# Kernel tuning notes

Measured on AMD Instinct MI355X. Metric: run time of the kernel, lower is better.

The kernel has to match this reference:

```python
import jax, jax.numpy as jnp
import numpy as np
from jax import lax

D, H_HEADS, DEPTH, E, HID, P, NCLS = 768, 12, 12, 4, 3072, 16, 1000

def _ln(x, w, b, eps=1e-5):
    m = x.mean(-1, keepdims=True)
    v = ((x - m) ** 2).mean(-1, keepdims=True)
    return (x - m) * lax.rsqrt(v + eps) * w + b

def setup_inputs() -> dict:
    key = jax.random.key(0)
    ks = jax.random.split(key, 16)
    s = 0.02
    inp = {
        'x': jax.random.normal(ks[0], (32, 3, 224, 224), jnp.float32),
        'conv_w': jax.random.normal(ks[1], (D, 3, P, P), jnp.float32) * s,
        'conv_b': jnp.zeros((D,), jnp.float32),
        'cls_token': jnp.zeros((1, 1, D), jnp.float32),
        'pos_embed': jax.random.normal(ks[2], (1, 197, D), jnp.float32) * s,
        'ln1_w': jnp.ones((DEPTH, D), jnp.float32),
        'ln1_b': jnp.zeros((DEPTH, D), jnp.float32),
        'qkv_w': jax.random.normal(ks[3], (DEPTH, 3 * D, D), jnp.float32) * s,
        'qkv_b': jnp.zeros((DEPTH, 3 * D), jnp.float32),
        'out_w': jax.random.normal(ks[4], (DEPTH, D, D), jnp.float32) * s,
        'out_b': jnp.zeros((DEPTH, D), jnp.float32),
        'ln2_w': jnp.ones((DEPTH, D), jnp.float32),
        'ln2_b': jnp.zeros((DEPTH, D), jnp.float32),
        'gate_w': jax.random.normal(ks[5], (DEPTH, E, D), jnp.float32) * s,
        'gate_b': jnp.zeros((DEPTH, E), jnp.float32),
        'e1_w': jax.random.normal(ks[6], (DEPTH, E, HID, D), jnp.float32) * s,
        'e1_b': jnp.zeros((DEPTH, E, HID), jnp.float32),
        'e2_w': jax.random.normal(ks[7], (DEPTH, E, D, HID), jnp.float32) * s,
        'e2_b': jnp.zeros((DEPTH, E, D), jnp.float32),
        'fnorm_w': jnp.ones((D,), jnp.float32),
        'fnorm_b': jnp.zeros((D,), jnp.float32),
        'head_w': jax.random.normal(ks[8], (NCLS, D), jnp.float32) * s,
        'head_b': jnp.zeros((NCLS,), jnp.float32),
    }
    return inp

def reference(x, conv_w, conv_b, cls_token, pos_embed, ln1_w, ln1_b, qkv_w, qkv_b,
              out_w, out_b, ln2_w, ln2_b, gate_w, gate_b, e1_w, e1_b, e2_w, e2_b,
              fnorm_w, fnorm_b, head_w, head_b):
    B = x.shape[0]
    # patch embedding: conv stride=patch, then flatten -> [B, N, D]
    x = lax.conv_general_dilated(x, conv_w, (P, P), 'VALID',
                                 dimension_numbers=('NCHW', 'OIHW', 'NCHW'))
    x = x + conv_b[None, :, None, None]
    x = x.reshape(B, D, -1).transpose(0, 2, 1)
    x = jnp.concatenate([jnp.broadcast_to(cls_token, (B, 1, D)), x], axis=1)
    x = x + pos_embed
    N = x.shape[1]
    hd = D // H_HEADS
    for i in range(DEPTH):
        # --- attention ---
        h = x
        y = _ln(x, ln1_w[i], ln1_b[i])
        qkv = y @ qkv_w[i].T + qkv_b[i]                      # [B,N,3D]
        q, k, v = jnp.split(qkv, 3, axis=-1)
        q = q.reshape(B, N, H_HEADS, hd).transpose(0, 2, 1, 3) / jnp.sqrt(hd).astype(x.dtype)
        k = k.reshape(B, N, H_HEADS, hd).transpose(0, 2, 1, 3)
        v = v.reshape(B, N, H_HEADS, hd).transpose(0, 2, 1, 3)
        attn = jax.nn.softmax(jnp.einsum('bhqd,bhkd->bhqk', q, k), axis=-1)
        ctx = jnp.einsum('bhqk,bhkd->bhqd', attn, v).transpose(0, 2, 1, 3).reshape(B, N, D)
        x = h + (ctx @ out_w[i].T + out_b[i])
        # --- MoE MLP (dense: all experts computed then masked, top_k=1) ---
        h = x
        y = _ln(x, ln2_w[i], ln2_b[i])
        gate = y @ gate_w[i].T + gate_b[i]                   # [B,N,E]
        topk_scores, topk_idx = lax.top_k(gate, 1)           # [B,N,1]
        score = jax.nn.softmax(topk_scores, axis=-1)[..., 0]  # [B,N] (==1 for k=1)
        h1 = jax.nn.gelu(jnp.einsum('bnd,ehd->benh', y, e1_w[i])
                         + e1_b[i][None, :, None, :], approximate=False)  # [B,E,N,HID]
        oe = jnp.einsum('benh,edh->bend', h1, e2_w[i]) + e2_b[i][None, :, None, :]
        mask = jax.nn.one_hot(topk_idx[..., 0], E, dtype=y.dtype)  # [B,N,E]
        moe = jnp.einsum('bne,bend->bnd', mask * score[..., None], oe)
        x = h + moe
    x = _ln(x, fnorm_w, fnorm_b)
    cls = x[:, 0]
    return cls @ head_w.T + head_b
```

## Files before the change

kernel.cpp:

```cpp
#include <hip/hip_runtime.h>
#include <hip/hip_bf16.h>
#include <math.h>

#define D_MODEL 768
#define SEQ     197
#define BATCH   32
#define NTOK    (BATCH*SEQ)
#define NHEAD   12
#define HDIM    64
#define NEXP    4
#define HID_N   3072
#define DEPTH_N 12

typedef __attribute__((ext_vector_type(4))) float f32x4;
typedef __attribute__((ext_vector_type(8))) short bf16x8;
typedef __attribute__((ext_vector_type(4))) unsigned short u16x4;
typedef unsigned short u16;

static __device__ __forceinline__ u16 f2bf(float f){
  unsigned int u = __builtin_bit_cast(unsigned int, f);
  u += 0x7FFFu + ((u >> 16) & 1u);
  return (u16)(u >> 16);
}
static __device__ __forceinline__ void split_bf(float x, u16& h, u16& l){
  h = f2bf(x);
  float hf = __builtin_bit_cast(float, (unsigned)h << 16);
  l = f2bf(x - hf);
}

static __device__ __forceinline__ float wred_sum(float v){
  #pragma unroll
  for (int off = 32; off; off >>= 1) v += __shfl_down(v, off);
  return v;
}

static __device__ __forceinline__ int xcd_map(int orig, int nwg){
  int q = nwg >> 3, r = nwg & 7;
  int xcd = orig & 7, idx = orig >> 3;
  return (xcd < r ? xcd*(q+1) : r*(q+1) + (xcd-r)*q) + idx;
}

static __device__ __forceinline__ void gld16(const u16* g, u16* l){
  __builtin_amdgcn_global_load_lds(
      (const __attribute__((address_space(1))) unsigned int*)g,
      (__attribute__((address_space(3))) unsigned int*)l, 16, 0, 0);
}

__global__ __launch_bounds__(256) void split_many(const float* __restrict__ src,
                                                  u16* __restrict__ hi,
                                                  u16* __restrict__ lo, long n4){
  for (long i = blockIdx.x*256L + threadIdx.x; i < n4; i += (long)gridDim.x*256){
    f32x4 v = *reinterpret_cast<const f32x4*>(src + i*4);
    u16x4 h, l;
    #pragma unroll
    for (int j = 0; j < 4; j++){ u16 hh, ll; split_bf(v[j], hh, ll); h[j]=hh; l[j]=ll; }
    *reinterpret_cast<u16x4*>(hi + i*4) = h;
    *reinterpret_cast<u16x4*>(lo + i*4) = l;
  }
}

template<int MODE>
__global__ __launch_bounds__(256, 2) void gemm_split(
    const u16* __restrict__ Ahp, const u16* __restrict__ Alp,
    const u16* __restrict__ Whp, const u16* __restrict__ Wlp,
    const float* __restrict__ bias, const float* __restrict__ resid,
    float* __restrict__ C, const float* __restrict__ pos,
    u16* __restrict__ Chi, u16* __restrict__ Clo,
    const int* __restrict__ toks, const int* __restrict__ cnts,
    const int* __restrict__ offs, const int* __restrict__ tiles,
    int M, int N, int K)
{
  const int tid = threadIdx.x;
  const int NB = N >> 7;
  const int nm = gridDim.x / NB;
  const int lg = xcd_map(blockIdx.x, gridDim.x);
  const int mt = lg % nm, nb = lg / nm;

  int cnt = M, base = 0, m0;
  if (MODE == 2 || MODE == 3){
    if (mt >= tiles[0]) return;
    const int e = tiles[1 + 2*mt];
    m0 = tiles[2 + 2*mt];
    cnt  = cnts[e];
    base = offs[e];
    Whp  += (size_t)e * N * K;
    Wlp  += (size_t)e * N * K;
    bias += (size_t)e * N;
  } else {
    m0 = mt * 128;
  }
  const int n0 = nb * 128;

  __shared__ __align__(16) u16 lds[2][4][4096];

  const int lane = tid & 63, wid = tid >> 6;
  const int i0 = wid*128 + lane;
  const int r0 = i0 >> 2, r1 = r0 + 16;
  const int x0 = (i0 & 3) ^ ((r0 >> 1) & 3);
  const int x1 = (i0 & 3) ^ ((r1 >> 1) & 3);
  const int d0 = wid*1024, d1 = wid*1024 + 512;

  size_t aA0 = 0, aA1 = 0, pb0 = 0, pb1 = 0;
  {
    const int gm0 = m0 + r0, gm1 = m0 + r1;
    if (MODE == 0 || MODE == 1){
      aA0 = (size_t)(gm0 < M ? gm0 : 0) * K + x0*8;
      aA1 = (size_t)(gm1 < M ? gm1 : 0) * K + x1*8;
    }
    if (MODE == 2){
      aA0 = (size_t)(gm0 < cnt ? toks[base+gm0] : 0) * K + x0*8;
      aA1 = (size_t)(gm1 < cnt ? toks[base+gm1] : 0) * K + x1*8;
    }
    if (MODE == 3){
      aA0 = (size_t)(gm0 < cnt ? base+gm0 : 0) * K + x0*8;
      aA1 = (size_t)(gm1 < cnt ? base+gm1 : 0) * K + x1*8;
    }
    if (MODE == 4){
      int b_ = gm0 / 196, pp = gm0 - b_*196;
      pb0 = (size_t)b_*150528 + (size_t)(pp/14)*3584 + (size_t)(pp%14)*16;
      b_ = gm1 / 196; pp = gm1 - b_*196;
      pb1 = (size_t)b_*150528 + (size_t)(pp/14)*3584 + (size_t)(pp%14)*16;
    }
  }
  const size_t aW0 = (size_t)(n0 + r0) * K + x0*8;
  const size_t aW1 = (size_t)(n0 + r1) * K + x1*8;

  auto STAGE = [&](int buf, int t){
    const int k0 = t * 32;
    if (MODE == 4){
      const int kq0 = k0 + x0*8, kq1 = k0 + x1*8;
      size_t a0 = pb0 + (size_t)(kq0>>8)*50176 + (size_t)((kq0>>4)&15)*224 + (size_t)(kq0&15);
      size_t a1 = pb1 + (size_t)(kq1>>8)*50176 + (size_t)((kq1>>4)&15)*224 + (size_t)(kq1&15);
      gld16(Ahp + a0, &lds[buf][0][d0]); gld16(Ahp + a1, &lds[buf][0][d1]);
      gld16(Alp + a0, &lds[buf][1][d0]); gld16(Alp + a1, &lds[buf][1][d1]);
    } else {
      gld16(Ahp + aA0 + k0, &lds[buf][0][d0]); gld16(Ahp + aA1 + k0, &lds[buf][0][d1]);
      gld16(Alp + aA0 + k0, &lds[buf][1][d0]); gld16(Alp + aA1 + k0, &lds[buf][1][d1]);
    }
    gld16(Whp + aW0 + k0, &lds[buf][2][d0]); gld16(Whp + aW1 + k0, &lds[buf][2][d1]);
    gld16(Wlp + aW0 + k0, &lds[buf][3][d0]); gld16(Wlp + aW1 + k0, &lds[buf][3][d1]);
  };

  const int wr = wid >> 1, wc = wid & 1;
  const int lr = lane & 15, lq = lane >> 4;
  int cA[4], cW[4];
  #pragma unroll
  for (int mi = 0; mi < 4; mi++){
    int ra = wr*64 + mi*16 + lr;
    cA[mi] = (4*ra + (lq ^ ((ra>>1)&3))) * 8;
  }
  #pragma unroll
  for (int nj = 0; nj < 4; nj++){
    int rw = wc*64 + nj*16 + lr;
    cW[nj] = (4*rw + (lq ^ ((rw>>1)&3))) * 8;
  }

  const int NT = K >> 5;
  f32x4 acc[4][4] = {};

  STAGE(0, 0);
  for (int t = 0; t < NT; t++){
    const int buf = t & 1;
    if (t + 1 < NT){
      STAGE(buf ^ 1, t + 1);
      asm volatile("s_waitcnt vmcnt(8)" ::: "memory");
    } else {
      asm volatile("s_waitcnt vmcnt(0)" ::: "memory");
    }
    __builtin_amdgcn_s_barrier();
    asm volatile("" ::: "memory");
    const u16* L = &lds[buf][0][0];
    bf16x8 afh[4], afl[4], bfh[4], bfl[4];
    #pragma unroll
    for (int mi = 0; mi < 4; mi++){
      afh[mi] = *reinterpret_cast<const bf16x8*>(L + cA[mi]);
      afl[mi] = *reinterpret_cast<const bf16x8*>(L + 4096 + cA[mi]);
    }
    #pragma unroll
    for (int nj = 0; nj < 4; nj++){
      bfh[nj] = *reinterpret_cast<const bf16x8*>(L + 2*4096 + cW[nj]);
      bfl[nj] = *reinterpret_cast<const bf16x8*>(L + 3*4096 + cW[nj]);
    }
    #pragma unroll
    for (int mi = 0; mi < 4; mi++)
      #pragma unroll
      for (int nj = 0; nj < 4; nj++){
        acc[mi][nj] = __builtin_amdgcn_mfma_f32_16x16x32_bf16(afh[mi], bfh[nj], acc[mi][nj], 0, 0, 0);
        acc[mi][nj] = __builtin_amdgcn_mfma_f32_16x16x32_bf16(afh[mi], bfl[nj], acc[mi][nj], 0, 0, 0);
        acc[mi][nj] = __builtin_amdgcn_mfma_f32_16x16x32_bf16(afl[mi], bfh[nj], acc[mi][nj], 0, 0, 0);
      }
    asm volatile("" ::: "memory");
    __builtin_amdgcn_s_barrier();
  }

  #pragma unroll
  for (int nj = 0; nj < 4; nj++){
    const int ncol = n0 + wc*64 + nj*16 + lr;
    const float bv = bias[ncol];
    #pragma unroll
    for (int mi = 0; mi < 4; mi++){
      const int mb = m0 + wr*64 + mi*16 + lq*4;
      #pragma unroll
      for (int j = 0; j < 4; j++){
        const int m = mb + j;
        float v = acc[mi][nj][j] + bv;
        if (MODE == 0){
          if (m < M) C[(size_t)m * N + ncol] = v;
        }
        if (MODE == 1){
          if (m < M) C[(size_t)m * N + ncol] = v + resid[(size_t)m * N + ncol];
        }
        if (MODE == 2){
          if (m < cnt){
            v = 0.5f * v * (1.f + erff(v * 0.70710678118f));
            u16 h, l; split_bf(v, h, l);
            Chi[(size_t)(base + m) * N + ncol] = h;
            Clo[(size_t)(base + m) * N + ncol] = l;
          }
        }
        if (MODE == 3){
          if (m < cnt){
            int tok = toks[base + m];
            C[(size_t)tok * N + ncol] += v;
          }
        }
        if (MODE == 4){
          int b_ = m / 196, pp = m - b_ * 196;
          C[((size_t)b_ * 197 + 1 + pp) * D_MODEL + ncol] =
              v + pos[(size_t)(1 + pp) * D_MODEL + ncol];
        }
      }
    }
  }
}

__global__ __launch_bounds__(256) void cls_init(const float* __restrict__ cls_tk,
                                                const float* __restrict__ pos,
                                                float* __restrict__ xt){
  const int b = blockIdx.x, tid = threadIdx.x;
  for (int d = tid; d < D_MODEL; d += 256)
    xt[((size_t)b*SEQ)*D_MODEL + d] = cls_tk[d] + pos[d];
}

__global__ __launch_bounds__(256) void ln_kernel(const float* __restrict__ x, size_t xstride,
                                                 const float* __restrict__ w,
                                                 const float* __restrict__ b,
                                                 float* __restrict__ y, size_t ystride,
                                                 u16* __restrict__ yh, u16* __restrict__ yl){
  const int t = blockIdx.x;
  const int tid = threadIdx.x;
  const float* row = x + (size_t)t*xstride;
  float v0 = row[tid], v1 = row[tid+256], v2 = row[tid+512];
  __shared__ float red[4];
  float s = wred_sum(v0+v1+v2);
  if ((tid & 63) == 0) red[tid>>6] = s;
  __syncthreads();
  const float mean = (red[0]+red[1]+red[2]+red[3]) * (1.f/768.f);
  const float d0 = v0-mean, d1 = v1-mean, d2 = v2-mean;
  __syncthreads();
  float q = wred_sum(d0*d0 + d1*d1 + d2*d2);
  if ((tid & 63) == 0) red[tid>>6] = q;
  __syncthreads();
  const float var = (red[0]+red[1]+red[2]+red[3]) * (1.f/768.f);
  const float inv = rsqrtf(var + 1e-5f);
  float o0 = d0*inv*w[tid]     + b[tid];
  float o1 = d1*inv*w[tid+256] + b[tid+256];
  float o2 = d2*inv*w[tid+512] + b[tid+512];
  float* yr = y + (size_t)t*ystride;
  yr[tid] = o0; yr[tid+256] = o1; yr[tid+512] = o2;
  if (yh){
    u16 h, l;
    size_t rb = (size_t)t*768;
    split_bf(o0, h, l); yh[rb+tid]     = h; yl[rb+tid]     = l;
    split_bf(o1, h, l); yh[rb+tid+256] = h; yl[rb+tid+256] = l;
    split_bf(o2, h, l); yh[rb+tid+512] = h; yl[rb+tid+512] = l;
  }
}

__global__ __launch_bounds__(256, 3) void attn_f32(const float* __restrict__ qkv,
                                                   u16* __restrict__ ctxh,
                                                   u16* __restrict__ ctxl){
  const int qt = blockIdx.x, h = blockIdx.y, b = blockIdx.z;
  const int tid = threadIdx.x;
  const int tx = tid & 15, ty = tid >> 4;
  __shared__ float Qs[64][65];
  __shared__ float KPs[64][65];
  __shared__ float Vs[64][65];
  const size_t rs = 3*D_MODEL;
  const float* base = qkv + (size_t)b*SEQ*rs + (size_t)h*HDIM;

  #pragma unroll
  for (int it = 0; it < 16; it++){
    int idx = tid + it*256;
    int r = idx >> 6, c = idx & 63;
    int gq = qt*64 + r;
    float v = (gq < SEQ) ? base[(size_t)gq*rs + c] : 0.f;
    Qs[r][c] = v * 0.125f;
  }
  float m_run[4], l_run[4], o[4][4];
  #pragma unroll
  for (int i = 0; i < 4; i++){
    m_run[i] = -3.0e38f; l_run[i] = 0.f;
    #pragma unroll
    for (int j = 0; j < 4; j++) o[i][j] = 0.f;
  }
  __syncthreads();

  for (int kt = 0; kt < 4; kt++){
    #pragma unroll
    for (int it = 0; it < 16; it++){
      int idx = tid + it*256;
      int r = idx >> 6, c = idx & 63;
      int gk = kt*64 + r;
      float kv = (gk < SEQ) ? base[(size_t)gk*rs + D_MODEL   + c] : 0.f;
      float vv = (gk < SEQ) ? base[(size_t)gk*rs + 2*D_MODEL + c] : 0.f;
      KPs[r][c] = kv;
      Vs[r][c]  = vv;
    }
    __syncthreads();
    float s[4][4] = {};
    for (int d = 0; d < 64; d++){
      float qv[4], kv2[4];
      #pragma unroll
      for (int i = 0; i < 4; i++) qv[i]  = Qs[ty*4+i][d];
      #pragma unroll
      for (int j = 0; j < 4; j++) kv2[j] = KPs[tx*4+j][d];
      #pragma unroll
      for (int i = 0; i < 4; i++)
        #pragma unroll
        for (int j = 0; j < 4; j++) s[i][j] += qv[i]*kv2[j];
    }
    #pragma unroll
    for (int j = 0; j < 4; j++){
      if (kt*64 + tx*4 + j >= SEQ){
        #pragma unroll
        for (int i = 0; i < 4; i++) s[i][j] = -3.0e38f;
      }
    }
    float scale[4];
    #pragma unroll
    for (int i = 0; i < 4; i++){
      float mt = fmaxf(fmaxf(s[i][0], s[i][1]), fmaxf(s[i][2], s[i][3]));
      #pragma unroll
      for (int msk = 1; msk <= 8; msk <<= 1) mt = fmaxf(mt, __shfl_xor(mt, msk));
      float mnew = fmaxf(m_run[i], mt);
      scale[i] = __expf(m_run[i] - mnew);
      float ls = 0.f;
      #pragma unroll
      for (int j = 0; j < 4; j++){ s[i][j] = __expf(s[i][j] - mnew); ls += s[i][j]; }
      #pragma unroll
      for (int msk = 1; msk <= 8; msk <<= 1) ls += __shfl_xor(ls, msk);
      l_run[i] = l_run[i]*scale[i] + ls;
      m_run[i] = mnew;
    }
    __syncthreads();
    #pragma unroll
    for (int i = 0; i < 4; i++)
      #pragma unroll
      for (int j = 0; j < 4; j++) KPs[ty*4+i][tx*4+j] = s[i][j];
    __syncthreads();
    #pragma unroll
    for (int i = 0; i < 4; i++)
      #pragma unroll
      for (int j = 0; j < 4; j++) o[i][j] *= scale[i];
    for (int k = 0; k < 64; k++){
      float pv[4], vv[4];
      #pragma unroll
      for (int i = 0; i < 4; i++) pv[i] = KPs[ty*4+i][k];
      #pragma unroll
      for (int j = 0; j < 4; j++) vv[j] = Vs[k][tx*4+j];
      #pragma unroll
      for (int i = 0; i < 4; i++)
        #pragma unroll
        for (int j = 0; j < 4; j++) o[i][j] += pv[i]*vv[j];
    }
    __syncthreads();
  }
  #pragma unroll
  for (int i = 0; i < 4; i++){
    int q = qt*64 + ty*4 + i;
    if (q < SEQ){
      float inv = 1.f / l_run[i];
      #pragma unroll
      for (int j = 0; j < 4; j++){
        u16 hh, ll;
        split_bf(o[i][j]*inv, hh, ll);
        size_t idx = ((size_t)(b*SEQ + q))*D_MODEL + h*HDIM + tx*4 + j;
        ctxh[idx] = hh; ctxl[idx] = ll;
      }
    }
  }
}

__global__ __launch_bounds__(256) void gate_kernel(const float* __restrict__ y,
                                                   const float* __restrict__ gw,
                                                   const float* __restrict__ gb,
                                                   int* __restrict__ eidx){
  const int t = blockIdx.x;
  const int tid = threadIdx.x;
  const int e = tid >> 6, lane = tid & 63;
  const float* row = y + (size_t)t*D_MODEL;
  const float* wrow = gw + (size_t)e*D_MODEL;
  float acc = 0.f;
  for (int k = lane; k < D_MODEL; k += 64) acc += row[k]*wrow[k];
  acc = wred_sum(acc);
  __shared__ float sc[NEXP];
  if (lane == 0) sc[e] = acc + gb[e];
  __syncthreads();
  if (tid == 0){
    int best = 0; float bv = sc[0];
    #pragma unroll
    for (int k = 1; k < NEXP; k++) if (sc[k] > bv){ bv = sc[k]; best = k; }
    eidx[t] = best;
  }
}

__global__ void zero_counts(int* c){ if (threadIdx.x < 3*NEXP) c[threadIdx.x] = 0; }

__global__ __launch_bounds__(256) void count_kernel(const int* __restrict__ eidx, int* counts){
  int i = blockIdx.x*256 + threadIdx.x;
  if (i < NTOK) atomicAdd(&counts[eidx[i]], 1);
}

__global__ void offsets_kernel(const int* counts, int* offs, int* cursor, int* tiles){
  if (threadIdx.x == 0){
    int o = 0, n = 0;
    for (int e = 0; e < NEXP; e++){
      offs[e] = o; cursor[e] = o;
      for (int m0 = 0; m0 < counts[e]; m0 += 128){
        tiles[1+2*n] = e; tiles[2+2*n] = m0; n++;
      }
      o += counts[e];
    }
    tiles[0] = n;
  }
}

__global__ __launch_bounds__(256) void scatter_kernel(const int* __restrict__ eidx,
                                                      int* cursor, int* __restrict__ toks){
  int i = blockIdx.x*256 + threadIdx.x;
  if (i < NTOK){ int pos = atomicAdd(&cursor[eidx[i]], 1); toks[pos] = i; }
}

__global__ __launch_bounds__(256) void gemm_f32(const float* __restrict__ A,
                                                const float* __restrict__ W,
                                                const float* __restrict__ bias,
                                                const float* __restrict__ resid,
                                                float* __restrict__ C,
                                                int M, int N, int K){
  const int m0 = blockIdx.x*64, bn = blockIdx.y*64;
  const int tid = threadIdx.x;
  const int tx = tid & 15, ty = tid >> 4;
  __shared__ float As[16][65];
  __shared__ float Ws[16][65];
  float acc[4][4] = {};
  for (int k0 = 0; k0 < K; k0 += 16){
    #pragma unroll
    for (int i = 0; i < 4; i++){
      int idx = tid + i*256;
      int k = idx & 15, m = idx >> 4;
      As[k][m] = (m0+m < M) ? A[(size_t)(m0+m)*K + k0 + k] : 0.f;
      Ws[k][m] = (bn+m < N) ? W[(size_t)(bn+m)*K + k0 + k] : 0.f;
    }
    __syncthreads();
    #pragma unroll
    for (int kk = 0; kk < 16; kk++){
      float a0 = As[kk][ty*4+0], a1 = As[kk][ty*4+1], a2 = As[kk][ty*4+2], a3 = As[kk][ty*4+3];
      float w0 = Ws[kk][tx*4+0], w1 = Ws[kk][tx*4+1], w2 = Ws[kk][tx*4+2], w3 = Ws[kk][tx*4+3];
      acc[0][0] += a0*w0; acc[0][1] += a0*w1; acc[0][2] += a0*w2; acc[0][3] += a0*w3;
      acc[1][0] += a1*w0; acc[1][1] += a1*w1; acc[1][2] += a1*w2; acc[1][3] += a1*w3;
      acc[2][0] += a2*w0; acc[2][1] += a2*w1; acc[2][2] += a2*w2; acc[2][3] += a2*w3;
      acc[3][0] += a3*w0; acc[3][1] += a3*w1; acc[3][2] += a3*w2; acc[3][3] += a3*w3;
    }
    __syncthreads();
  }
  #pragma unroll
  for (int i = 0; i < 4; i++){
    int m = m0 + ty*4 + i;
    if (m >= M) continue;
    #pragma unroll
    for (int j = 0; j < 4; j++){
      int n = bn + tx*4 + j;
      if (n >= N) continue;
      float v = acc[i][j];
      if (bias)  v += bias[n];
      if (resid) v += resid[(size_t)m*N + n];
      C[(size_t)m*N + n] = v;
    }
  }
}

extern "C" void kernel_launch(void* const* d_in, const int* in_sizes, int n_in,
                              void* d_out, int out_size, void* d_ws, size_t ws_size,
                              hipStream_t stream){
  const float* x      = (const float*)d_in[0];
  const float* conv_w = (const float*)d_in[1];
  const float* conv_b = (const float*)d_in[2];
  const float* cls_tk = (const float*)d_in[3];
  const float* pos    = (const float*)d_in[4];
  const float* ln1w   = (const float*)d_in[5];
  const float* ln1b   = (const float*)d_in[6];
  const float* qkvw   = (const float*)d_in[7];
  const float* qkvb   = (const float*)d_in[8];
  const float* outw   = (const float*)d_in[9];
  const float* outb   = (const float*)d_in[10];
  const float* ln2w   = (const float*)d_in[11];
  const float* ln2b   = (const float*)d_in[12];
  const float* gatew  = (const float*)d_in[13];
  const float* gateb  = (const float*)d_in[14];
  const float* e1w    = (const float*)d_in[15];
  const float* e1b    = (const float*)d_in[16];
  const float* e2w    = (const float*)d_in[17];
  const float* e2b    = (const float*)d_in[18];
  const float* fnw    = (const float*)d_in[19];
  const float* fnb    = (const float*)d_in[20];
  const float* headw  = (const float*)d_in[21];
  const float* headb  = (const float*)d_in[22];
  float* out = (float*)d_out;

  float* ws    = (float*)d_ws;
  float* xt    = ws;
  float* y     = xt  + (size_t)NTOK*D_MODEL;
  float* qkv   = y   + (size_t)NTOK*D_MODEL;
  float* clsln = qkv + (size_t)NTOK*3*D_MODEL;
  int*   eidx   = (int*)(clsln + (size_t)BATCH*D_MODEL);
  int*   toks   = eidx + NTOK;
  int*   counts = toks + NTOK;
  int*   offs   = counts + NEXP;
  int*   cursor = offs + NEXP;
  int*   tiles  = cursor + NEXP;
  u16* up = (u16*)(((size_t)(tiles + 120) + 15) & ~(size_t)15);
  const size_t nY  = (size_t)NTOK*D_MODEL;
  const size_t nH1 = (size_t)NTOK*HID_N;
  const size_t nX  = (size_t)BATCH*3*224*224;
  const size_t nCW = 768*768;
  const size_t nQW = (size_t)DEPTH_N*3*D_MODEL*D_MODEL;
  const size_t nOW = (size_t)DEPTH_N*D_MODEL*D_MODEL;
  const size_t nE1 = (size_t)DEPTH_N*NEXP*HID_N*D_MODEL;
  const size_t nE2 = (size_t)DEPTH_N*NEXP*D_MODEL*HID_N;
  u16 *yh = up,      *yl = yh + nY;
  u16 *ch = yl + nY, *cl = ch + nY;
  u16 *h1h = cl + nY, *h1l = h1h + nH1;
  u16 *xh = h1l + nH1, *xl = xh + nX;
  u16 *cwh = xl + nX,  *cwl = cwh + nCW;
  u16 *qwh = cwl + nCW, *qwl = qwh + nQW;
  u16 *owh = qwl + nQW, *owl = owh + nOW;
  u16 *e1h = owl + nOW, *e1l = e1h + nE1;
  u16 *e2h = e1l + nE1, *e2l = e2h + nE2;

  dim3 b256(256);

  split_many<<<2048, b256, 0, stream>>>(x,      xh,  xl,  (long)(nX/4));
  split_many<<<2048, b256, 0, stream>>>(conv_w, cwh, cwl, (long)(nCW/4));
  split_many<<<2048, b256, 0, stream>>>(qkvw,   qwh, qwl, (long)(nQW/4));
  split_many<<<2048, b256, 0, stream>>>(outw,   owh, owl, (long)(nOW/4));
  split_many<<<2048, b256, 0, stream>>>(e1w,    e1h, e1l, (long)(nE1/4));
  split_many<<<2048, b256, 0, stream>>>(e2w,    e2h, e2l, (long)(nE2/4));

  gemm_split<4><<<dim3(49*6), b256, 0, stream>>>(xh, xl, cwh, cwl,
      conv_b, nullptr, xt, pos, nullptr, nullptr,
      nullptr, nullptr, nullptr, nullptr, 6272, D_MODEL, 768);
  cls_init<<<dim3(BATCH), b256, 0, stream>>>(cls_tk, pos, xt);

  for (int i = 0; i < DEPTH_N; i++){
    ln_kernel<<<dim3(NTOK), b256, 0, stream>>>(xt, D_MODEL,
        ln1w + (size_t)i*D_MODEL, ln1b + (size_t)i*D_MODEL, y, D_MODEL, yh, yl);
    gemm_split<0><<<dim3(50*18), b256, 0, stream>>>(yh, yl,
        qwh + (size_t)i*3*D_MODEL*D_MODEL, qwl + (size_t)i*3*D_MODEL*D_MODEL,
        qkvb + (size_t)i*3*D_MODEL, nullptr, qkv, nullptr, nullptr, nullptr,
        nullptr, nullptr, nullptr, nullptr, NTOK, 3*D_MODEL, D_MODEL);
    attn_f32<<<dim3(4, NHEAD, BATCH), b256, 0, stream>>>(qkv, ch, cl);
    gemm_split<1><<<dim3(50*6), b256, 0, stream>>>(ch, cl,
        owh + (size_t)i*D_MODEL*D_MODEL, owl + (size_t)i*D_MODEL*D_MODEL,
        outb + (size_t)i*D_MODEL, xt, xt, nullptr, nullptr, nullptr,
        nullptr, nullptr, nullptr, nullptr, NTOK, D_MODEL, D_MODEL);
    ln_kernel<<<dim3(NTOK), b256, 0, stream>>>(xt, D_MODEL,
        ln2w + (size_t)i*D_MODEL, ln2b + (size_t)i*D_MODEL, y, D_MODEL, yh, yl);
    gate_kernel<<<dim3(NTOK), b256, 0, stream>>>(y,
        gatew + (size_t)i*NEXP*D_MODEL, gateb + (size_t)i*NEXP, eidx);
    zero_counts<<<1, 64, 0, stream>>>(counts);
    count_kernel<<<dim3((NTOK+255)/256), b256, 0, stream>>>(eidx, counts);
    offsets_kernel<<<1, 64, 0, stream>>>(counts, offs, cursor, tiles);
    scatter_kernel<<<dim3((NTOK+255)/256), b256, 0, stream>>>(eidx, cursor, toks);
    gemm_split<2><<<dim3(53*(HID_N/128)), b256, 0, stream>>>(yh, yl,
        e1h + (size_t)i*NEXP*HID_N*D_MODEL, e1l + (size_t)i*NEXP*HID_N*D_MODEL,
        e1b + (size_t)i*NEXP*HID_N, nullptr, nullptr, nullptr, h1h, h1l,
        toks, counts, offs, tiles, NTOK, HID_N, D_MODEL);
    gemm_split<3><<<dim3(53*(D_MODEL/128)), b256, 0, stream>>>(h1h, h1l,
        e2h + (size_t)i*NEXP*D_MODEL*HID_N, e2l + (size_t)i*NEXP*D_MODEL*HID_N,
        e2b + (size_t)i*NEXP*D_MODEL, nullptr, xt, nullptr, nullptr, nullptr,
        toks, counts, offs, tiles, NTOK, D_MODEL, HID_N);
  }

  ln_kernel<<<dim3(BATCH), b256, 0, stream>>>(xt, (size_t)SEQ*D_MODEL, fnw, fnb,
      clsln, D_MODEL, nullptr, nullptr);
  gemm_f32<<<dim3(1, 16), b256, 0, stream>>>(clsln, headw, headb, nullptr, out, BATCH, 1000, D_MODEL);
}
```

Measured before the change: 11.10 ms.

## Single-buffer GEMM LDS for higher occupancy, reorder tiles, fuse expert counting into gate

The split-bf16 GEMM drops its LDS double buffer and async prefetch in favour of a single buffer with two block barriers per K step. It raises launch bounds to 4 blocks per CU, aiming to hide memory latency through occupancy rather than software pipelining. Tile rasterisation becomes N-major for every mode except the first expert GEMM, which changes L2 reuse of A versus W. The per-token expert count is folded into the gate kernel via an atomic, removing one kernel launch per layer, at the cost of serialising load and compute within each block.

```diff
diff --git a/kernel.cpp b/kernel.cpp
--- a/kernel.cpp
+++ b/kernel.cpp
@@ -60,7 +60,7 @@
 }
 
 template<int MODE>
-__global__ __launch_bounds__(256, 2) void gemm_split(
+__global__ __launch_bounds__(256, 4) void gemm_split(
     const u16* __restrict__ Ahp, const u16* __restrict__ Alp,
     const u16* __restrict__ Whp, const u16* __restrict__ Wlp,
     const float* __restrict__ bias, const float* __restrict__ resid,
@@ -74,7 +74,9 @@
   const int NB = N >> 7;
   const int nm = gridDim.x / NB;
   const int lg = xcd_map(blockIdx.x, gridDim.x);
-  const int mt = lg % nm, nb = lg / nm;
+  int mt, nb;
+  if (MODE == 2){ mt = lg % nm; nb = lg / nm; }
+  else          { nb = lg % NB; mt = lg / NB; }
 
   int cnt = M, base = 0, m0;
   if (MODE == 2 || MODE == 3){
@@ -91,7 +93,7 @@
   }
   const int n0 = nb * 128;
 
-  __shared__ __align__(16) u16 lds[2][4][4096];
+  __shared__ __align__(16) u16 lds[4][4096];
 
   const int lane = tid & 63, wid = tid >> 6;
   const int i0 = wid*128 + lane;
@@ -125,20 +127,20 @@
   const size_t aW0 = (size_t)(n0 + r0) * K + x0*8;
   const size_t aW1 = (size_t)(n0 + r1) * K + x1*8;
 
-  auto STAGE = [&](int buf, int t){
+  auto STAGE = [&](int t){
     const int k0 = t * 32;
     if (MODE == 4){
       const int kq0 = k0 + x0*8, kq1 = k0 + x1*8;
       size_t a0 = pb0 + (size_t)(kq0>>8)*50176 + (size_t)((kq0>>4)&15)*224 + (size_t)(kq0&15);
       size_t a1 = pb1 + (size_t)(kq1>>8)*50176 + (size_t)((kq1>>4)&15)*224 + (size_t)(kq1&15);
-      gld16(Ahp + a0, &lds[buf][0][d0]); gld16(Ahp + a1, &lds[buf][0][d1]);
-      gld16(Alp + a0, &lds[buf][1][d0]); gld16(Alp + a1, &lds[buf][1][d1]);
+      gld16(Ahp + a0, &lds[0][d0]); gld16(Ahp + a1, &lds[0][d1]);
+      gld16(Alp + a0, &lds[1][d0]); gld16(Alp + a1, &lds[1][d1]);
     } else {
-      gld16(Ahp + aA0 + k0, &lds[buf][0][d0]); gld16(Ahp + aA1 + k0, &lds[buf][0][d1]);
-      gld16(Alp + aA0 + k0, &lds[buf][1][d0]); gld16(Alp + aA1 + k0, &lds[buf][1][d1]);
-    }
-    gld16(Whp + aW0 + k0, &lds[buf][2][d0]); gld16(Whp + aW1 + k0, &lds[buf][2][d1]);
-    gld16(Wlp + aW0 + k0, &lds[buf][3][d0]); gld16(Wlp + aW1 + k0, &lds[buf][3][d1]);
+      gld16(Ahp + aA0 + k0, &lds[0][d0]); gld16(Ahp + aA1 + k0, &lds[0][d1]);
+      gld16(Alp + aA0 + k0, &lds[1][d0]); gld16(Alp + aA1 + k0, &lds[1][d1]);
+    }
+    gld16(Whp + aW0 + k0, &lds[2][d0]); gld16(Whp + aW1 + k0, &lds[2][d1]);
+    gld16(Wlp + aW0 + k0, &lds[3][d0]); gld16(Wlp + aW1 + k0, &lds[3][d1]);
   };
 
   const int wr = wid >> 1, wc = wid & 1;
@@ -158,18 +160,11 @@
   const int NT = K >> 5;
   f32x4 acc[4][4] = {};
 
-  STAGE(0, 0);
   for (int t = 0; t < NT; t++){
-    const int buf = t & 1;
-    if (t + 1 < NT){
-      STAGE(buf ^ 1, t + 1);
-      asm volatile("s_waitcnt vmcnt(8)" ::: "memory");
-    } else {
-      asm volatile("s_waitcnt vmcnt(0)" ::: "memory");
-    }
-    __builtin_amdgcn_s_barrier();
-    asm volatile("" ::: "memory");
-    const u16* L = &lds[buf][0][0];
+    if (t) __syncthreads();
+    STAGE(t);
+    __syncthreads();
+    const u16* L = &lds[0][0];
     bf16x8 afh[4], afl[4], bfh[4], bfl[4];
     #pragma unroll
     for (int mi = 0; mi < 4; mi++){
@@ -189,8 +184,6 @@
         acc[mi][nj] = __builtin_amdgcn_mfma_f32_16x16x32_bf16(afh[mi], bfl[nj], acc[mi][nj], 0, 0, 0);
         acc[mi][nj] = __builtin_amdgcn_mfma_f32_16x16x32_bf16(afl[mi], bfh[nj], acc[mi][nj], 0, 0, 0);
       }
-    asm volatile("" ::: "memory");
-    __builtin_amdgcn_s_barrier();
   }
 
   #pragma unroll
@@ -395,7 +388,8 @@
 __global__ __launch_bounds__(256) void gate_kernel(const float* __restrict__ y,
                                                    const float* __restrict__ gw,
                                                    const float* __restrict__ gb,
-                                                   int* __restrict__ eidx){
+                                                   int* __restrict__ eidx,
+                                                   int* __restrict__ counts){
   const int t = blockIdx.x;
   const int tid = threadIdx.x;
   const int e = tid >> 6, lane = tid & 63;
@@ -412,15 +406,11 @@
     #pragma unroll
     for (int k = 1; k < NEXP; k++) if (sc[k] > bv){ bv = sc[k]; best = k; }
     eidx[t] = best;
+    atomicAdd(&counts[best], 1);
   }
 }
 
 __global__ void zero_counts(int* c){ if (threadIdx.x < 3*NEXP) c[threadIdx.x] = 0; }
-
-__global__ __launch_bounds__(256) void count_kernel(const int* __restrict__ eidx, int* counts){
-  int i = blockIdx.x*256 + threadIdx.x;
-  if (i < NTOK) atomicAdd(&counts[eidx[i]], 1);
-}
 
 __global__ void offsets_kernel(const int* counts, int* offs, int* cursor, int* tiles){
   if (threadIdx.x == 0){
@@ -576,10 +566,9 @@
         nullptr, nullptr, nullptr, nullptr, NTOK, D_MODEL, D_MODEL);
     ln_kernel<<<dim3(NTOK), b256, 0, stream>>>(xt, D_MODEL,
         ln2w + (size_t)i*D_MODEL, ln2b + (size_t)i*D_MODEL, y, D_MODEL, yh, yl);
+    zero_counts<<<1, 64, 0, stream>>>(counts);
     gate_kernel<<<dim3(NTOK), b256, 0, stream>>>(y,
-        gatew + (size_t)i*NEXP*D_MODEL, gateb + (size_t)i*NEXP, eidx);
-    zero_counts<<<1, 64, 0, stream>>>(counts);
-    count_kernel<<<dim3((NTOK+255)/256), b256, 0, stream>>>(eidx, counts);
+        gatew + (size_t)i*NEXP*D_MODEL, gateb + (size_t)i*NEXP, eidx, counts);
     offsets_kernel<<<1, 64, 0, stream>>>(counts, offs, cursor, tiles);
     scatter_kernel<<<dim3((NTOK+255)/256), b256, 0, stream>>>(eidx, cursor, toks);
     gemm_split<2><<<dim3(53*(HID_N/128)), b256, 0, stream>>>(yh, yl,
```

After: 11.40 ms. 2.6% more time.
